# Optimization experiments

Hardware: AMD Instinct MI355X
Metric: run time of the kernel (lower is better)

Reference implementation:

```python
import jax, jax.numpy as jnp
import numpy as np

STATE_DIM = 64
HIDDEN_DIM = 256
BATCH = 4096
DT = 0.01


def setup_inputs() -> dict:
    key = jax.random.key(0)
    ks = jax.random.split(key, 7)
    s = 1.0 / np.sqrt(STATE_DIM)
    h = 1.0 / np.sqrt(HIDDEN_DIM)
    return {
        "x0": jax.random.normal(ks[0], (BATCH, STATE_DIM), dtype=jnp.float32),
        "W1": jax.random.uniform(ks[1], (STATE_DIM, HIDDEN_DIM), jnp.float32, -s, s),
        "b1": jax.random.uniform(ks[2], (HIDDEN_DIM,), jnp.float32, -s, s),
        "W2": jax.random.uniform(ks[3], (HIDDEN_DIM, HIDDEN_DIM), jnp.float32, -h, h),
        "b2": jax.random.uniform(ks[4], (HIDDEN_DIM,), jnp.float32, -h, h),
        "W3": jax.random.uniform(ks[5], (HIDDEN_DIM, STATE_DIM), jnp.float32, -h, h),
        "b3": jax.random.uniform(ks[6], (STATE_DIM,), jnp.float32, -h, h),
        "dt_scale": jnp.ones((1,), dtype=jnp.float32) * 0.01,
        "steps": 200,
    }


def reference(x0, W1, b1, W2, b2, W3, b3, dt_scale, steps):
    def func(x):
        h1 = jnp.tanh(x @ W1 + b1)
        h2 = jnp.tanh(h1 @ W2 + b2)
        return h2 @ W3 + b3

    def step(x, _):
        x_next = x + func(x) * dt_scale * DT  # Euler update
        return x_next, x_next

    _, traj = jax.lax.scan(step, x0, None, length=steps)
    # traj: [steps, batch, state_dim] -> [batch, steps+1, state_dim]
    return jnp.concatenate([x0[:, None, :], jnp.swapaxes(traj, 0, 1)], axis=1)
```

## Files before the change

### kernel.cpp

```cpp
#include <hip/hip_runtime.h>


#define STATE_DIM 64
#define HIDDEN    256
#define TILE_M    16
#define NBLK      256
#define XPITCH    72
#define HPITCH    264
#define XSP       68

typedef short v8s __attribute__((ext_vector_type(8)));
typedef float v4f __attribute__((ext_vector_type(4)));

__device__ __forceinline__ unsigned short f2bf(float f) {
    return (unsigned short)((__float_as_uint(f) + 0x8000u) >> 16);
}

__device__ __forceinline__ float fast_tanh(float x) {
    float e = __builtin_amdgcn_exp2f(x * 2.8853900817779268f);
    return 1.0f - 2.0f * __builtin_amdgcn_rcpf(e + 1.0f);
}

__global__ void prep_weights(const float* __restrict__ W1,
                             const float* __restrict__ W2,
                             const float* __restrict__ W3,
                             short* __restrict__ W1t,
                             short* __restrict__ W2t,
                             short* __restrict__ W3t) {
    int u = blockIdx.x * 256 + threadIdx.x;
    if (u < 65536) {
        int n = u >> 8, k = u & 255;
        W2t[u] = (short)f2bf(W2[k * 256 + n]);
    }
    int v = u - 65536;
    if (v >= 0 && v < 16384) {
        int n = v >> 6, k = v & 63;
        W1t[v] = (short)f2bf(W1[k * 256 + n]);
    }
    int t = u - (65536 + 16384);
    if (t >= 0 && t < 16384) {
        int n = t >> 8, k = t & 255;
        W3t[t] = (short)f2bf(W3[k * 64 + n]);
    }
}

__global__ __launch_bounds__(512, 2)
void ode_kernel(const float* __restrict__ x0,
                const float* __restrict__ b1,
                const float* __restrict__ b2,
                const float* __restrict__ b3,
                const float* __restrict__ dt_scale,
                const int*   __restrict__ stepsp,
                const short* __restrict__ W1t,
                const short* __restrict__ W2t,
                const short* __restrict__ W3t,
                float* __restrict__ out) {
    __shared__ short xb [TILE_M * XPITCH];
    __shared__ short h1b[TILE_M * HPITCH];
    __shared__ short h2b[TILE_M * HPITCH];
    __shared__ float xs [2][TILE_M * XSP];

    const int tid  = threadIdx.x;
    const int w    = tid >> 6;
    const int lane = tid & 63;
    const int ln   = lane & 15;
    const int q    = lane >> 4;
    const int blk  = blockIdx.x;
    const int nsteps = *stepsp;
    const float scale = dt_scale[0] * 0.01f;
    const int n0 = 32 * w;

    v8s w1f[2][2], w2f[2][8], w3f[8];
    #pragma unroll
    for (int t = 0; t < 2; t++)
        #pragma unroll
        for (int ks = 0; ks < 2; ks++)
            w1f[t][ks] = *(const v8s*)(W1t + (n0 + 16 * t + ln) * 64 + 32 * ks + 8 * q);
    #pragma unroll
    for (int t = 0; t < 2; t++)
        #pragma unroll
        for (int ks = 0; ks < 8; ks++)
            w2f[t][ks] = *(const v8s*)(W2t + (n0 + 16 * t + ln) * 256 + 32 * ks + 8 * q);
    if (w < 4) {
        #pragma unroll
        for (int ks = 0; ks < 8; ks++)
            w3f[ks] = *(const v8s*)(W3t + (16 * w + ln) * 256 + 32 * ks + 8 * q);
    }
    float b1r[2], b2r[2], b3r = 0.0f;
    #pragma unroll
    for (int t = 0; t < 2; t++) {
        b1r[t] = b1[n0 + 16 * t + ln];
        b2r[t] = b2[n0 + 16 * t + ln];
    }
    if (w < 4) b3r = b3[16 * w + ln];

    {
        int r = tid >> 5, c = (tid & 31) * 2;
        const float2 v = *(const float2*)(x0 + (size_t)(blk * TILE_M + r) * STATE_DIM + c);
        xs[0][r * XSP + c]     = v.x;
        xs[0][r * XSP + c + 1] = v.y;
        xb[r * XPITCH + c]     = (short)f2bf(v.x);
        xb[r * XPITCH + c + 1] = (short)f2bf(v.y);
    }
    __syncthreads();

    int xrd[2], hrd[8], hw0, xsU[4], xbU[4];
    #pragma unroll
    for (int ks = 0; ks < 2; ks++) xrd[ks] = ln * XPITCH + 32 * ks + 8 * q;
    #pragma unroll
    for (int ks = 0; ks < 8; ks++) hrd[ks] = ln * HPITCH + 32 * ks + 8 * q;
    hw0 = (4 * q) * HPITCH + n0 + ln;
    {
        int col = 16 * (w & 3) + ln;
        #pragma unroll
        for (int i = 0; i < 4; i++) {
            xsU[i] = (4 * q + i) * XSP + col;
            xbU[i] = (4 * q + i) * XPITCH + col;
        }
    }

    const size_t orow = (size_t)(nsteps + 1) * STATE_DIM;
    float* tp[4];
    int trd[4];
    {
        int r0 = 4 * (w - 4);
        #pragma unroll
        for (int j = 0; j < 4; j++) {
            int r = (w >= 4) ? (r0 + j) : 0;
            tp[j]  = out + (size_t)(blk * TILE_M + r) * orow + lane;
            trd[j] = r * XSP + lane;
        }
    }

    for (int s = 0; s < nsteps; s++) {
        const int cur = s & 1, nxt = cur ^ 1;

        v8s xa0 = *(const v8s*)(xb + xrd[0]);
        v8s xa1 = *(const v8s*)(xb + xrd[1]);
        v4f acc0 = {0.f, 0.f, 0.f, 0.f}, acc1 = {0.f, 0.f, 0.f, 0.f};
        acc0 = __builtin_amdgcn_mfma_f32_16x16x32_bf16(xa0, w1f[0][0], acc0, 0, 0, 0);
        acc1 = __builtin_amdgcn_mfma_f32_16x16x32_bf16(xa0, w1f[1][0], acc1, 0, 0, 0);
        acc0 = __builtin_amdgcn_mfma_f32_16x16x32_bf16(xa1, w1f[0][1], acc0, 0, 0, 0);
        acc1 = __builtin_amdgcn_mfma_f32_16x16x32_bf16(xa1, w1f[1][1], acc1, 0, 0, 0);
        #pragma unroll
        for (int i = 0; i < 4; i++) {
            h1b[hw0 + i * HPITCH]      = (short)f2bf(fast_tanh(acc0[i] + b1r[0]));
            h1b[hw0 + i * HPITCH + 16] = (short)f2bf(fast_tanh(acc1[i] + b1r[1]));
        }
        __syncthreads();

        v8s a[8];
        #pragma unroll
        for (int ks = 0; ks < 8; ks++) a[ks] = *(const v8s*)(h1b + hrd[ks]);
        acc0 = (v4f){0.f, 0.f, 0.f, 0.f};
        acc1 = (v4f){0.f, 0.f, 0.f, 0.f};
        #pragma unroll
        for (int ks = 0; ks < 8; ks++) {
            acc0 = __builtin_amdgcn_mfma_f32_16x16x32_bf16(a[ks], w2f[0][ks], acc0, 0, 0, 0);
            acc1 = __builtin_amdgcn_mfma_f32_16x16x32_bf16(a[ks], w2f[1][ks], acc1, 0, 0, 0);
        }
        #pragma unroll
        for (int i = 0; i < 4; i++) {
            h2b[hw0 + i * HPITCH]      = (short)f2bf(fast_tanh(acc0[i] + b2r[0]));
            h2b[hw0 + i * HPITCH + 16] = (short)f2bf(fast_tanh(acc1[i] + b2r[1]));
        }
        __syncthreads();

        if (w < 4) {
            v8s c[8];
            #pragma unroll
            for (int ks = 0; ks < 8; ks++) c[ks] = *(const v8s*)(h2b + hrd[ks]);
            v4f a3 = {0.f, 0.f, 0.f, 0.f};
            #pragma unroll
            for (int ks = 0; ks < 8; ks++)
                a3 = __builtin_amdgcn_mfma_f32_16x16x32_bf16(c[ks], w3f[ks], a3, 0, 0, 0);
            #pragma unroll
            for (int i = 0; i < 4; i++) {
                float xn = xs[cur][xsU[i]] + (a3[i] + b3r) * scale;
                xs[nxt][xsU[i]] = xn;
                xb[xbU[i]] = (short)f2bf(xn);
            }
        } else {
            #pragma unroll
            for (int j = 0; j < 4; j++) {
                *tp[j] = xs[cur][trd[j]];
                tp[j] += STATE_DIM;
            }
        }
        __syncthreads();
    }

    {
        const float* xsf = xs[nsteps & 1];
        #pragma unroll
        for (int j = 0; j < 2; j++) {
            int r = 2 * w + j;
            out[(size_t)(blk * TILE_M + r) * orow + (size_t)nsteps * STATE_DIM + lane] =
                xsf[r * XSP + lane];
        }
    }
}

extern "C" void kernel_launch(void* const* d_in, const int* in_sizes, int n_in,
                              void* d_out, int out_size, void* d_ws, size_t ws_size,
                              hipStream_t stream) {
    const float* x0 = (const float*)d_in[0];
    const float* W1 = (const float*)d_in[1];
    const float* b1 = (const float*)d_in[2];
    const float* W2 = (const float*)d_in[3];
    const float* b2 = (const float*)d_in[4];
    const float* W3 = (const float*)d_in[5];
    const float* b3 = (const float*)d_in[6];
    const float* dt = (const float*)d_in[7];
    const int* steps = (const int*)d_in[8];

    short* W1t = (short*)d_ws;
    short* W2t = W1t + 64 * 256;
    short* W3t = W2t + 256 * 256;

    prep_weights<<<384, 256, 0, stream>>>(W1, W2, W3, W1t, W2t, W3t);
    ode_kernel<<<NBLK, 512, 0, stream>>>(x0, b1, b2, b3, dt, steps,
                                         W1t, W2t, W3t, (float*)d_out);
}
```

Before: 448.5 us.

## Swap MFMA operands to keep state in registers and vectorize LDS stores

Swaps the A/B operands of every MFMA so each lane's accumulator holds four consecutive hidden/state columns of one row. This allows packed bf16 uint2 stores to LDS, bias folding into the accumulator init, and keeping the fp32 state x in registers. The fp32 shared state double buffer and the separate trajectory-writer warps are removed, and the compute warps now write trajectory rows directly with 16-byte global stores. The Euler update is reduced to a single fmaf per element. In exchange, half the warps no longer do useful work in the final stage, and the output writes now sit on the critical path of the compute warps. LDS pitches also change.

```diff
diff --git a/kernel.cpp b/kernel.cpp
--- a/kernel.cpp
+++ b/kernel.cpp
@@ -5,9 +5,8 @@
 #define HIDDEN    256
 #define TILE_M    16
 #define NBLK      256
-#define XPITCH    72
-#define HPITCH    264
-#define XSP       68
+#define XPITCH    68
+#define HPITCH    260
 
 typedef short v8s __attribute__((ext_vector_type(8)));
 typedef float v4f __attribute__((ext_vector_type(4)));
@@ -15,7 +14,10 @@
 __device__ __forceinline__ unsigned short f2bf(float f) {
     return (unsigned short)((__float_as_uint(f) + 0x8000u) >> 16);
 }
-
+__device__ __forceinline__ unsigned pk2bf(float a, float b) {
+    return ((__float_as_uint(a) + 0x8000u) >> 16) |
+           ((__float_as_uint(b) + 0x8000u) & 0xffff0000u);
+}
 __device__ __forceinline__ float fast_tanh(float x) {
     float e = __builtin_amdgcn_exp2f(x * 2.8853900817779268f);
     return 1.0f - 2.0f * __builtin_amdgcn_rcpf(e + 1.0f);
@@ -58,7 +60,6 @@
     __shared__ short xb [TILE_M * XPITCH];
     __shared__ short h1b[TILE_M * HPITCH];
     __shared__ short h2b[TILE_M * HPITCH];
-    __shared__ float xs [2][TILE_M * XSP];
 
     const int tid  = threadIdx.x;
     const int w    = tid >> 6;
@@ -86,118 +87,91 @@
         for (int ks = 0; ks < 8; ks++)
             w3f[ks] = *(const v8s*)(W3t + (16 * w + ln) * 256 + 32 * ks + 8 * q);
     }
-    float b1r[2], b2r[2], b3r = 0.0f;
+    v4f b1v[2], b2v[2], b3v = {0.f, 0.f, 0.f, 0.f};
     #pragma unroll
     for (int t = 0; t < 2; t++) {
-        b1r[t] = b1[n0 + 16 * t + ln];
-        b2r[t] = b2[n0 + 16 * t + ln];
+        b1v[t] = *(const v4f*)(b1 + n0 + 16 * t + 4 * q);
+        b2v[t] = *(const v4f*)(b2 + n0 + 16 * t + 4 * q);
     }
-    if (w < 4) b3r = b3[16 * w + ln];
+    if (w < 4) b3v = *(const v4f*)(b3 + 16 * w + 4 * q);
 
-    {
-        int r = tid >> 5, c = (tid & 31) * 2;
-        const float2 v = *(const float2*)(x0 + (size_t)(blk * TILE_M + r) * STATE_DIM + c);
-        xs[0][r * XSP + c]     = v.x;
-        xs[0][r * XSP + c + 1] = v.y;
-        xb[r * XPITCH + c]     = (short)f2bf(v.x);
-        xb[r * XPITCH + c + 1] = (short)f2bf(v.y);
+    v4f x = {0.f, 0.f, 0.f, 0.f};
+    unsigned tbase = 0;
+    const int xw0 = ln * XPITCH + 16 * w + 4 * q;
+    if (w < 4) {
+        x = *(const v4f*)(x0 + (size_t)(blk * TILE_M + ln) * STATE_DIM + 16 * w + 4 * q);
+        uint2 p; p.x = pk2bf(x[0], x[1]); p.y = pk2bf(x[2], x[3]);
+        *(uint2*)(xb + xw0) = p;
+        tbase = (unsigned)(blk * TILE_M + ln) * (unsigned)((nsteps + 1) * STATE_DIM)
+              + 16 * w + 4 * q;
+        *(v4f*)(out + tbase) = x;
+        tbase += STATE_DIM;
     }
     __syncthreads();
 
-    int xrd[2], hrd[8], hw0, xsU[4], xbU[4];
+    int xrd[2], hrd[8];
     #pragma unroll
     for (int ks = 0; ks < 2; ks++) xrd[ks] = ln * XPITCH + 32 * ks + 8 * q;
     #pragma unroll
     for (int ks = 0; ks < 8; ks++) hrd[ks] = ln * HPITCH + 32 * ks + 8 * q;
-    hw0 = (4 * q) * HPITCH + n0 + ln;
-    {
-        int col = 16 * (w & 3) + ln;
-        #pragma unroll
-        for (int i = 0; i < 4; i++) {
-            xsU[i] = (4 * q + i) * XSP + col;
-            xbU[i] = (4 * q + i) * XPITCH + col;
-        }
-    }
-
-    const size_t orow = (size_t)(nsteps + 1) * STATE_DIM;
-    float* tp[4];
-    int trd[4];
-    {
-        int r0 = 4 * (w - 4);
-        #pragma unroll
-        for (int j = 0; j < 4; j++) {
-            int r = (w >= 4) ? (r0 + j) : 0;
-            tp[j]  = out + (size_t)(blk * TILE_M + r) * orow + lane;
-            trd[j] = r * XSP + lane;
-        }
-    }
+    const int hw0 = ln * HPITCH + n0 + 4 * q;
 
     for (int s = 0; s < nsteps; s++) {
-        const int cur = s & 1, nxt = cur ^ 1;
-
         v8s xa0 = *(const v8s*)(xb + xrd[0]);
         v8s xa1 = *(const v8s*)(xb + xrd[1]);
-        v4f acc0 = {0.f, 0.f, 0.f, 0.f}, acc1 = {0.f, 0.f, 0.f, 0.f};
-        acc0 = __builtin_amdgcn_mfma_f32_16x16x32_bf16(xa0, w1f[0][0], acc0, 0, 0, 0);
-        acc1 = __builtin_amdgcn_mfma_f32_16x16x32_bf16(xa0, w1f[1][0], acc1, 0, 0, 0);
-        acc0 = __builtin_amdgcn_mfma_f32_16x16x32_bf16(xa1, w1f[0][1], acc0, 0, 0, 0);
-        acc1 = __builtin_amdgcn_mfma_f32_16x16x32_bf16(xa1, w1f[1][1], acc1, 0, 0, 0);
-        #pragma unroll
-        for (int i = 0; i < 4; i++) {
-            h1b[hw0 + i * HPITCH]      = (short)f2bf(fast_tanh(acc0[i] + b1r[0]));
-            h1b[hw0 + i * HPITCH + 16] = (short)f2bf(fast_tanh(acc1[i] + b1r[1]));
+        v4f a0 = b1v[0], a1 = b1v[1];
+        a0 = __builtin_amdgcn_mfma_f32_16x16x32_bf16(w1f[0][0], xa0, a0, 0, 0, 0);
+        a1 = __builtin_amdgcn_mfma_f32_16x16x32_bf16(w1f[1][0], xa0, a1, 0, 0, 0);
+        a0 = __builtin_amdgcn_mfma_f32_16x16x32_bf16(w1f[0][1], xa1, a0, 0, 0, 0);
+        a1 = __builtin_amdgcn_mfma_f32_16x16x32_bf16(w1f[1][1], xa1, a1, 0, 0, 0);
+        {
+            uint2 p0, p1;
+            p0.x = pk2bf(fast_tanh(a0[0]), fast_tanh(a0[1]));
+            p0.y = pk2bf(fast_tanh(a0[2]), fast_tanh(a0[3]));
+            p1.x = pk2bf(fast_tanh(a1[0]), fast_tanh(a1[1]));
+            p1.y = pk2bf(fast_tanh(a1[2]), fast_tanh(a1[3]));
+            *(uint2*)(h1b + hw0)      = p0;
+            *(uint2*)(h1b + hw0 + 16) = p1;
         }
         __syncthreads();
 
-        v8s a[8];
+        v8s ha[8];
         #pragma unroll
-        for (int ks = 0; ks < 8; ks++) a[ks] = *(const v8s*)(h1b + hrd[ks]);
-        acc0 = (v4f){0.f, 0.f, 0.f, 0.f};
-        acc1 = (v4f){0.f, 0.f, 0.f, 0.f};
+        for (int ks = 0; ks < 8; ks++) ha[ks] = *(const v8s*)(h1b + hrd[ks]);
+        a0 = b2v[0]; a1 = b2v[1];
         #pragma unroll
         for (int ks = 0; ks < 8; ks++) {
-            acc0 = __builtin_amdgcn_mfma_f32_16x16x32_bf16(a[ks], w2f[0][ks], acc0, 0, 0, 0);
-            acc1 = __builtin_amdgcn_mfma_f32_16x16x32_bf16(a[ks], w2f[1][ks], acc1, 0, 0, 0);
+            a0 = __builtin_amdgcn_mfma_f32_16x16x32_bf16(w2f[0][ks], ha[ks], a0, 0, 0, 0);
+            a1 = __builtin_amdgcn_mfma_f32_16x16x32_bf16(w2f[1][ks], ha[ks], a1, 0, 0, 0);
         }
-        #pragma unroll
-        for (int i = 0; i < 4; i++) {
-            h2b[hw0 + i * HPITCH]      = (short)f2bf(fast_tanh(acc0[i] + b2r[0]));
-            h2b[hw0 + i * HPITCH + 16] = (short)f2bf(fast_tanh(acc1[i] + b2r[1]));
+        {
+            uint2 p0, p1;
+            p0.x = pk2bf(fast_tanh(a0[0]), fast_tanh(a0[1]));
+            p0.y = pk2bf(fast_tanh(a0[2]), fast_tanh(a0[3]));
+            p1.x = pk2bf(fast_tanh(a1[0]), fast_tanh(a1[1]));
+            p1.y = pk2bf(fast_tanh(a1[2]), fast_tanh(a1[3]));
+            *(uint2*)(h2b + hw0)      = p0;
+            *(uint2*)(h2b + hw0 + 16) = p1;
         }
         __syncthreads();
 
         if (w < 4) {
-            v8s c[8];
+            v8s hc[8];
             #pragma unroll
-            for (int ks = 0; ks < 8; ks++) c[ks] = *(const v8s*)(h2b + hrd[ks]);
-            v4f a3 = {0.f, 0.f, 0.f, 0.f};
+            for (int ks = 0; ks < 8; ks++) hc[ks] = *(const v8s*)(h2b + hrd[ks]);
+            v4f a3 = b3v;
             #pragma unroll
             for (int ks = 0; ks < 8; ks++)
-                a3 = __builtin_amdgcn_mfma_f32_16x16x32_bf16(c[ks], w3f[ks], a3, 0, 0, 0);
+                a3 = __builtin_amdgcn_mfma_f32_16x16x32_bf16(w3f[ks], hc[ks], a3, 0, 0, 0);
             #pragma unroll
-            for (int i = 0; i < 4; i++) {
-                float xn = xs[cur][xsU[i]] + (a3[i] + b3r) * scale;
-                xs[nxt][xsU[i]] = xn;
-                xb[xbU[i]] = (short)f2bf(xn);
-            }
-        } else {
-            #pragma unroll
-            for (int j = 0; j < 4; j++) {
-                *tp[j] = xs[cur][trd[j]];
-                tp[j] += STATE_DIM;
-            }
+            for (int i = 0; i < 4; i++)
+                x[i] = fmaf(a3[i], scale, x[i]);
+            uint2 p; p.x = pk2bf(x[0], x[1]); p.y = pk2bf(x[2], x[3]);
+            *(uint2*)(xb + xw0) = p;
+            *(v4f*)(out + tbase) = x;
+            tbase += STATE_DIM;
         }
         __syncthreads();
-    }
-
-    {
-        const float* xsf = xs[nsteps & 1];
-        #pragma unroll
-        for (int j = 0; j < 2; j++) {
-            int r = 2 * w + j;
-            out[(size_t)(blk * TILE_M + r) * orow + (size_t)nsteps * STATE_DIM + lane] =
-                xsf[r * XSP + lane];
-        }
     }
 }
 
```

Result: faster. 430.2 us (-4.1%).
